# Performance work log

Measured on AMD Instinct MI355X. Metric: run time of the kernel, lower is better.

The kernel has to match this reference:

```python
import jax, jax.numpy as jnp
import numpy as np

N_QUBITS = 4
N_LAYERS = 6
BATCH = 262144


def _apply_1q(state, U, wire):
    """Apply a 1-qubit gate U ((2,2) shared or (B,2,2) per-sample) on `wire`.
    state: (B, 2, 2, ..., 2) with n qubit axes after the batch axis."""
    s = jnp.moveaxis(state, 1 + wire, -1)
    shp = s.shape
    s2 = s.reshape(shp[0], -1, 2)
    if U.ndim == 3:
        s2 = jnp.einsum('bij,bkj->bki', U, s2)
    else:
        s2 = jnp.einsum('ij,bkj->bki', U, s2)
    return jnp.moveaxis(s2.reshape(shp), -1, 1 + wire)


def _apply_cnot(state, control, target):
    s = jnp.moveaxis(state, (1 + control, 1 + target), (-2, -1))
    shp = s.shape
    s2 = s.reshape(shp[0], -1, 2, 2)
    # flip target amplitudes where control bit is 1
    s2 = jnp.stack([s2[..., 0, :], s2[..., 1, ::-1]], axis=-2)
    return jnp.moveaxis(s2.reshape(shp), (-2, -1), (1 + control, 1 + target))


def _ry_batched(x):
    """RY(x) for x: (B,) -> (B,2,2) complex64 (real-valued matrix)."""
    c, s = jnp.cos(x / 2), jnp.sin(x / 2)
    m = jnp.stack([jnp.stack([c, -s], -1), jnp.stack([s, c], -1)], -2)
    return m.astype(jnp.complex64)


def _rot(phi, theta, omega):
    """qml.Rot = RZ(omega) RY(theta) RZ(phi), (2,2) complex64."""
    c, s = jnp.cos(theta / 2), jnp.sin(theta / 2)
    e = lambda a: jnp.exp(1j * a)
    m00 = e(-(phi + omega) / 2) * c
    m01 = -e((phi - omega) / 2) * s
    m10 = e(-(phi - omega) / 2) * s
    m11 = e((phi + omega) / 2) * c
    return jnp.stack([jnp.stack([m00, m01]), jnp.stack([m10, m11])]).astype(jnp.complex64)


def setup_inputs() -> dict:
    key = jax.random.key(0)
    k1, k2 = jax.random.split(key)
    inputs = jax.random.normal(k1, (BATCH, N_QUBITS), dtype=jnp.float32)
    quantum_weights = jax.random.uniform(k2, (N_LAYERS, N_QUBITS, 3), dtype=jnp.float32, minval=-0.05, maxval=0.05)
    return {"inputs": inputs, "quantum_weights": quantum_weights}


def reference(inputs, quantum_weights):
    B, n = inputs.shape
    L = quantum_weights.shape[0]
    # |0...0> state, batched
    state = jnp.zeros((B,) + (2,) * n, jnp.complex64)
    state = state.at[(slice(None),) + (0,) * n].set(1.0)
    # AngleEmbedding(rotation='Y'): RY(inputs[:, w]) on wire w
    for w in range(n):
        state = _apply_1q(state, _ry_batched(inputs[:, w]), w)
    # StronglyEntanglingLayers: Rot per wire, then ring of CNOTs with range r = l % (n-1) + 1
    for l in range(L):
        for w in range(n):
            state = _apply_1q(state, _rot(quantum_weights[l, w, 0], quantum_weights[l, w, 1], quantum_weights[l, w, 2]), w)
        r = l % (n - 1) + 1
        for w in range(n):
            state = _apply_cnot(state, w, (w + r) % n)
    # <Z_w> for each wire
    p = jnp.abs(state.reshape(B, -1)) ** 2  # (B, 2^n)
    bits = (jnp.arange(2 ** n)[:, None] >> jnp.arange(n - 1, -1, -1)[None, :]) & 1
    z = (1 - 2 * bits).astype(p.dtype)  # (2^n, n)
    return p @ z  # (B, n) float32
```

## Files before the change

### kernel.cpp

```cpp
#include <hip/hip_runtime.h>

#define N_QUBITS 4
#define N_LAYERS 6
#define NSTATES  16

__device__ __forceinline__ float2 cmul(float2 a, float2 b) {
    return make_float2(a.x * b.x - a.y * b.y, a.x * b.y + a.y * b.x);
}
__device__ __forceinline__ float2 cadd(float2 a, float2 b) {
    return make_float2(a.x + b.x, a.y + b.y);
}

__global__ __launch_bounds__(256) void build_u_kernel(
        const float* __restrict__ weights, float* __restrict__ U) {
    __shared__ float2 rotm[N_LAYERS * N_QUBITS][4];
    __shared__ float2 st[NSTATES][NSTATES];

    const int t = threadIdx.x;
    if (t < N_LAYERS * N_QUBITS) {
        const float phi   = weights[t * 3 + 0];
        const float theta = weights[t * 3 + 1];
        const float omega = weights[t * 3 + 2];
        float stheta, ctheta;
        sincosf(theta * 0.5f, &stheta, &ctheta);
        const float a1 = -(phi + omega) * 0.5f;
        const float a2 =  (phi - omega) * 0.5f;
        float s1, c1, s2, c2;
        sincosf(a1, &s1, &c1);
        sincosf(a2, &s2, &c2);
        rotm[t][0] = make_float2( c1 * ctheta,  s1 * ctheta);
        rotm[t][1] = make_float2(-c2 * stheta, -s2 * stheta);
        rotm[t][2] = make_float2( c2 * stheta, -s2 * stheta);
        rotm[t][3] = make_float2( c1 * ctheta, -s1 * ctheta);
    }

    const int c = t >> 4;
    const int i = t & 15;
    st[c][i] = make_float2(i == c ? 1.0f : 0.0f, 0.0f);
    __syncthreads();

    #pragma unroll 1
    for (int l = 0; l < N_LAYERS; ++l) {
        #pragma unroll 1
        for (int w = 0; w < N_QUBITS; ++w) {
            const int bit = 8 >> w;
            if (!(i & bit)) {
                const int j = i | bit;
                const float2 a0 = st[c][i];
                const float2 a1v = st[c][j];
                const float2 m00 = rotm[l * N_QUBITS + w][0];
                const float2 m01 = rotm[l * N_QUBITS + w][1];
                const float2 m10 = rotm[l * N_QUBITS + w][2];
                const float2 m11 = rotm[l * N_QUBITS + w][3];
                st[c][i] = cadd(cmul(m00, a0), cmul(m01, a1v));
                st[c][j] = cadd(cmul(m10, a0), cmul(m11, a1v));
            }
            __syncthreads();
        }
        const int r = l % (N_QUBITS - 1) + 1;
        int fi = i;
        #pragma unroll
        for (int w = 0; w < N_QUBITS; ++w) {
            const int tb = 8 >> ((w + r) & 3);
            if ((fi >> (3 - w)) & 1) fi ^= tb;
        }
        const float2 a = st[c][i];
        __syncthreads();
        st[c][fi] = a;
        __syncthreads();
    }

    U[2 * (i * NSTATES + c) + 0] = st[c][i].x;
    U[2 * (i * NSTATES + c) + 1] = st[c][i].y;
}

__global__ __launch_bounds__(256) void qc_apply_kernel(
        const float* __restrict__ inputs,
        const float* __restrict__ U,
        float* __restrict__ out,
        int B) {
    const int b = blockIdx.x * blockDim.x + threadIdx.x;
    if (b >= B) return;

    const float4 xin = reinterpret_cast<const float4*>(inputs)[b];
    float s0, c0, s1, c1, s2, c2, s3, c3;
    __sincosf(xin.x * 0.5f, &s0, &c0);
    __sincosf(xin.y * 0.5f, &s1, &c1);
    __sincosf(xin.z * 0.5f, &s2, &c2);
    __sincosf(xin.w * 0.5f, &s3, &c3);

    const float vA[4] = { c0 * c1, c0 * s1, s0 * c1, s0 * s1 };
    const float vB[4] = { c2 * c3, c2 * s3, s2 * c3, s2 * s3 };
    float v[NSTATES];
    #pragma unroll
    for (int a = 0; a < 4; ++a)
        #pragma unroll
        for (int q = 0; q < 4; ++q)
            v[a * 4 + q] = vA[a] * vB[q];

    float p[NSTATES];
    #pragma unroll
    for (int i = 0; i < NSTATES; ++i) {
        const float4* row = reinterpret_cast<const float4*>(U + 2 * NSTATES * i);
        float re = 0.0f, im = 0.0f;
        #pragma unroll
        for (int q = 0; q < 8; ++q) {
            const float4 u4 = row[q];
            re = fmaf(u4.x, v[2 * q],     re);
            im = fmaf(u4.y, v[2 * q],     im);
            re = fmaf(u4.z, v[2 * q + 1], re);
            im = fmaf(u4.w, v[2 * q + 1], im);
        }
        p[i] = re * re + im * im;
    }

    float sa[8], da[8];
    #pragma unroll
    for (int j = 0; j < 8; ++j) {
        sa[j] = p[2 * j] + p[2 * j + 1];
        da[j] = p[2 * j] - p[2 * j + 1];
    }
    const float z3 = ((da[0] + da[1]) + (da[2] + da[3])) +
                     ((da[4] + da[5]) + (da[6] + da[7]));
    float sb[4], db[4];
    #pragma unroll
    for (int j = 0; j < 4; ++j) {
        sb[j] = sa[2 * j] + sa[2 * j + 1];
        db[j] = sa[2 * j] - sa[2 * j + 1];
    }
    const float z2 = (db[0] + db[1]) + (db[2] + db[3]);
    const float z1 = (sb[0] - sb[1]) + (sb[2] - sb[3]);
    const float z0 = (sb[0] + sb[1]) - (sb[2] + sb[3]);

    reinterpret_cast<float4*>(out)[b] = make_float4(z0, z1, z2, z3);
}

extern "C" void kernel_launch(void* const* d_in, const int* in_sizes, int n_in,
                              void* d_out, int out_size, void* d_ws, size_t ws_size,
                              hipStream_t stream) {
    const float* inputs  = (const float*)d_in[0];
    const float* weights = (const float*)d_in[1];
    float* out = (float*)d_out;
    float* U   = (float*)d_ws;
    const int B = in_sizes[0] / N_QUBITS;

    build_u_kernel<<<1, 256, 0, stream>>>(weights, U);

    const int block = 256;
    const int grid = (B + block - 1) / block;
    qc_apply_kernel<<<grid, block, 0, stream>>>(inputs, U, out, B);
}
```

Measured before the change: 68.34 us.

## Fuse unitary construction into apply kernel, recomputing U per block in LDS

Removes the separate single-block kernel that built the 16x16 circuit unitary and had it written to global memory. Every block of the main kernel now rebuilds the unitary in shared memory (about 24 gate steps with barriers) and reads it from LDS with broadcast float4 loads. This saves one launch and the serialised dependency between the two kernels. The cost is redundant per-block gate simulation across 1024 blocks plus many __syncthreads before the main work begins.

```diff
diff --git a/kernel.cpp b/kernel.cpp
--- a/kernel.cpp
+++ b/kernel.cpp
@@ -11,12 +11,16 @@
     return make_float2(a.x + b.x, a.y + b.y);
 }
 
-__global__ __launch_bounds__(256) void build_u_kernel(
-        const float* __restrict__ weights, float* __restrict__ U) {
+__global__ __launch_bounds__(256) void qc_fused_kernel(
+        const float* __restrict__ inputs,
+        const float* __restrict__ weights,
+        float* __restrict__ out,
+        int B) {
     __shared__ float2 rotm[N_LAYERS * N_QUBITS][4];
-    __shared__ float2 st[NSTATES][NSTATES];
+    __shared__ __align__(16) float2 st[NSTATES][NSTATES];
 
     const int t = threadIdx.x;
+
     if (t < N_LAYERS * N_QUBITS) {
         const float phi   = weights[t * 3 + 0];
         const float theta = weights[t * 3 + 1];
@@ -46,7 +50,7 @@
             const int bit = 8 >> w;
             if (!(i & bit)) {
                 const int j = i | bit;
-                const float2 a0 = st[c][i];
+                const float2 a0  = st[c][i];
                 const float2 a1v = st[c][j];
                 const float2 m00 = rotm[l * N_QUBITS + w][0];
                 const float2 m01 = rotm[l * N_QUBITS + w][1];
@@ -70,16 +74,7 @@
         __syncthreads();
     }
 
-    U[2 * (i * NSTATES + c) + 0] = st[c][i].x;
-    U[2 * (i * NSTATES + c) + 1] = st[c][i].y;
-}
-
-__global__ __launch_bounds__(256) void qc_apply_kernel(
-        const float* __restrict__ inputs,
-        const float* __restrict__ U,
-        float* __restrict__ out,
-        int B) {
-    const int b = blockIdx.x * blockDim.x + threadIdx.x;
+    const int b = blockIdx.x * blockDim.x + t;
     if (b >= B) return;
 
     const float4 xin = reinterpret_cast<const float4*>(inputs)[b];
@@ -98,21 +93,28 @@
         for (int q = 0; q < 4; ++q)
             v[a * 4 + q] = vA[a] * vB[q];
 
+    float2 amp[NSTATES];
+    #pragma unroll
+    for (int q = 0; q < NSTATES; ++q) amp[q] = make_float2(0.0f, 0.0f);
+
+    #pragma unroll
+    for (int k = 0; k < NSTATES; ++k) {
+        const float vk = v[k];
+        const float4* col = reinterpret_cast<const float4*>(&st[k][0]);
+        #pragma unroll
+        for (int j = 0; j < 8; ++j) {
+            const float4 u4 = col[j];
+            amp[2 * j].x     = fmaf(vk, u4.x, amp[2 * j].x);
+            amp[2 * j].y     = fmaf(vk, u4.y, amp[2 * j].y);
+            amp[2 * j + 1].x = fmaf(vk, u4.z, amp[2 * j + 1].x);
+            amp[2 * j + 1].y = fmaf(vk, u4.w, amp[2 * j + 1].y);
+        }
+    }
+
     float p[NSTATES];
     #pragma unroll
-    for (int i = 0; i < NSTATES; ++i) {
-        const float4* row = reinterpret_cast<const float4*>(U + 2 * NSTATES * i);
-        float re = 0.0f, im = 0.0f;
-        #pragma unroll
-        for (int q = 0; q < 8; ++q) {
-            const float4 u4 = row[q];
-            re = fmaf(u4.x, v[2 * q],     re);
-            im = fmaf(u4.y, v[2 * q],     im);
-            re = fmaf(u4.z, v[2 * q + 1], re);
-            im = fmaf(u4.w, v[2 * q + 1], im);
-        }
-        p[i] = re * re + im * im;
-    }
+    for (int q = 0; q < NSTATES; ++q)
+        p[q] = amp[q].x * amp[q].x + amp[q].y * amp[q].y;
 
     float sa[8], da[8];
     #pragma unroll
@@ -141,12 +143,9 @@
     const float* inputs  = (const float*)d_in[0];
     const float* weights = (const float*)d_in[1];
     float* out = (float*)d_out;
-    float* U   = (float*)d_ws;
     const int B = in_sizes[0] / N_QUBITS;
-
-    build_u_kernel<<<1, 256, 0, stream>>>(weights, U);
 
     const int block = 256;
     const int grid = (B + block - 1) / block;
-    qc_apply_kernel<<<grid, block, 0, stream>>>(inputs, U, out, B);
+    qc_fused_kernel<<<grid, block, 0, stream>>>(inputs, weights, out, B);
 }
```

New measurement: 92.71 us. 1.36x slower.

## Build circuit unitary in registers per column and drop barriers

Applied to the files above, without the earlier changes.

The unitary build kernel now has each of 16 threads evolve one column entirely in registers with fully unrolled gates and CNOT permutations, replacing the 256-thread shared-memory version that synchronised after every gate. The apply kernel gets a compile-time no-guard variant when the batch divides by 256, and it accumulates the Z expectations directly instead of using a butterfly reduction. The aim is to shorten the serial single-block build kernel, which sits on the critical path before the main kernel. The cost is more register pressure and code size in that build kernel.

```diff
diff --git a/kernel.cpp b/kernel.cpp
--- a/kernel.cpp
+++ b/kernel.cpp
@@ -11,10 +11,9 @@
     return make_float2(a.x + b.x, a.y + b.y);
 }
 
-__global__ __launch_bounds__(256) void build_u_kernel(
+__global__ __launch_bounds__(64) void build_u_kernel(
         const float* __restrict__ weights, float* __restrict__ U) {
     __shared__ float2 rotm[N_LAYERS * N_QUBITS][4];
-    __shared__ float2 st[NSTATES][NSTATES];
 
     const int t = threadIdx.x;
     if (t < N_LAYERS * N_QUBITS) {
@@ -33,54 +32,64 @@
         rotm[t][2] = make_float2( c2 * stheta, -s2 * stheta);
         rotm[t][3] = make_float2( c1 * ctheta, -s1 * ctheta);
     }
-
-    const int c = t >> 4;
-    const int i = t & 15;
-    st[c][i] = make_float2(i == c ? 1.0f : 0.0f, 0.0f);
     __syncthreads();
 
-    #pragma unroll 1
-    for (int l = 0; l < N_LAYERS; ++l) {
-        #pragma unroll 1
-        for (int w = 0; w < N_QUBITS; ++w) {
-            const int bit = 8 >> w;
-            if (!(i & bit)) {
-                const int j = i | bit;
-                const float2 a0 = st[c][i];
-                const float2 a1v = st[c][j];
+    if (t < NSTATES) {
+        const int c = t;
+        float2 s[NSTATES];
+        #pragma unroll
+        for (int q = 0; q < NSTATES; ++q)
+            s[q] = make_float2(q == c ? 1.0f : 0.0f, 0.0f);
+
+        #pragma unroll
+        for (int l = 0; l < N_LAYERS; ++l) {
+            #pragma unroll
+            for (int w = 0; w < N_QUBITS; ++w) {
                 const float2 m00 = rotm[l * N_QUBITS + w][0];
                 const float2 m01 = rotm[l * N_QUBITS + w][1];
                 const float2 m10 = rotm[l * N_QUBITS + w][2];
                 const float2 m11 = rotm[l * N_QUBITS + w][3];
-                st[c][i] = cadd(cmul(m00, a0), cmul(m01, a1v));
-                st[c][j] = cadd(cmul(m10, a0), cmul(m11, a1v));
+                const int bit = 8 >> w;
+                #pragma unroll
+                for (int i = 0; i < NSTATES; ++i) {
+                    if (i & bit) continue;
+                    const int j = i | bit;
+                    const float2 a0 = s[i];
+                    const float2 a1v = s[j];
+                    s[i] = cadd(cmul(m00, a0), cmul(m01, a1v));
+                    s[j] = cadd(cmul(m10, a0), cmul(m11, a1v));
+                }
             }
-            __syncthreads();
+            const int r = l % (N_QUBITS - 1) + 1;
+            float2 tmp[NSTATES];
+            #pragma unroll
+            for (int i = 0; i < NSTATES; ++i) {
+                int fi = i;
+                #pragma unroll
+                for (int w = 0; w < N_QUBITS; ++w) {
+                    const int tb = 8 >> ((w + r) & 3);
+                    if ((fi >> (3 - w)) & 1) fi ^= tb;
+                }
+                tmp[fi] = s[i];
+            }
+            #pragma unroll
+            for (int i = 0; i < NSTATES; ++i) s[i] = tmp[i];
         }
-        const int r = l % (N_QUBITS - 1) + 1;
-        int fi = i;
+
         #pragma unroll
-        for (int w = 0; w < N_QUBITS; ++w) {
-            const int tb = 8 >> ((w + r) & 3);
-            if ((fi >> (3 - w)) & 1) fi ^= tb;
-        }
-        const float2 a = st[c][i];
-        __syncthreads();
-        st[c][fi] = a;
-        __syncthreads();
+        for (int i = 0; i < NSTATES; ++i)
+            reinterpret_cast<float2*>(U)[i * NSTATES + c] = s[i];
     }
-
-    U[2 * (i * NSTATES + c) + 0] = st[c][i].x;
-    U[2 * (i * NSTATES + c) + 1] = st[c][i].y;
 }
 
+template<bool GUARD>
 __global__ __launch_bounds__(256) void qc_apply_kernel(
         const float* __restrict__ inputs,
         const float* __restrict__ U,
         float* __restrict__ out,
         int B) {
-    const int b = blockIdx.x * blockDim.x + threadIdx.x;
-    if (b >= B) return;
+    const int b = blockIdx.x * 256 + threadIdx.x;
+    if (GUARD && b >= B) return;
 
     const float4 xin = reinterpret_cast<const float4*>(inputs)[b];
     float s0, c0, s1, c1, s2, c2, s3, c3;
@@ -98,7 +107,7 @@
         for (int q = 0; q < 4; ++q)
             v[a * 4 + q] = vA[a] * vB[q];
 
-    float p[NSTATES];
+    float z0 = 0.0f, z1 = 0.0f, z2 = 0.0f, z3 = 0.0f;
     #pragma unroll
     for (int i = 0; i < NSTATES; ++i) {
         const float4* row = reinterpret_cast<const float4*>(U + 2 * NSTATES * i);
@@ -111,26 +120,12 @@
             re = fmaf(u4.z, v[2 * q + 1], re);
             im = fmaf(u4.w, v[2 * q + 1], im);
         }
-        p[i] = re * re + im * im;
+        const float p = re * re + im * im;
+        z0 = (i & 8) ? z0 - p : z0 + p;
+        z1 = (i & 4) ? z1 - p : z1 + p;
+        z2 = (i & 2) ? z2 - p : z2 + p;
+        z3 = (i & 1) ? z3 - p : z3 + p;
     }
-
-    float sa[8], da[8];
-    #pragma unroll
-    for (int j = 0; j < 8; ++j) {
-        sa[j] = p[2 * j] + p[2 * j + 1];
-        da[j] = p[2 * j] - p[2 * j + 1];
-    }
-    const float z3 = ((da[0] + da[1]) + (da[2] + da[3])) +
-                     ((da[4] + da[5]) + (da[6] + da[7]));
-    float sb[4], db[4];
-    #pragma unroll
-    for (int j = 0; j < 4; ++j) {
-        sb[j] = sa[2 * j] + sa[2 * j + 1];
-        db[j] = sa[2 * j] - sa[2 * j + 1];
-    }
-    const float z2 = (db[0] + db[1]) + (db[2] + db[3]);
-    const float z1 = (sb[0] - sb[1]) + (sb[2] - sb[3]);
-    const float z0 = (sb[0] + sb[1]) - (sb[2] + sb[3]);
 
     reinterpret_cast<float4*>(out)[b] = make_float4(z0, z1, z2, z3);
 }
@@ -144,9 +139,11 @@
     float* U   = (float*)d_ws;
     const int B = in_sizes[0] / N_QUBITS;
 
-    build_u_kernel<<<1, 256, 0, stream>>>(weights, U);
+    build_u_kernel<<<1, 64, 0, stream>>>(weights, U);
 
-    const int block = 256;
-    const int grid = (B + block - 1) / block;
-    qc_apply_kernel<<<grid, block, 0, stream>>>(inputs, U, out, B);
+    if ((B & 255) == 0) {
+        qc_apply_kernel<false><<<B / 256, 256, 0, stream>>>(inputs, U, out, B);
+    } else {
+        qc_apply_kernel<true><<<(B + 255) / 256, 256, 0, stream>>>(inputs, U, out, B);
+    }
 }
```

Measured after the change: 70.10 us. 2.6% more time.
